# Performance work log

Measured on AMD Instinct MI355X. Metric: run time of the kernel, lower is better.

The kernel has to match this reference:

```python
import jax, jax.numpy as jnp
import numpy as np

B, C, H, W = 2, 256, 64, 64
HEADS, DIM_HEAD = 8, 64
INNER = HEADS * DIM_HEAD


def setup_inputs() -> dict:
    key = jax.random.key(0)
    k1, k2, k3, k4 = jax.random.split(key, 4)
    x = jax.random.normal(k1, (B, C, H, W), dtype=jnp.float32)
    # 1x1 conv weights stored as [out_ch, in_ch]
    w_qkv = jax.random.normal(k2, (3 * INNER, C), dtype=jnp.float32) * (1.0 / np.sqrt(C))
    w_out = jax.random.normal(k3, (C, INNER), dtype=jnp.float32) * (1.0 / np.sqrt(INNER))
    b_out = jax.random.normal(k4, (C,), dtype=jnp.float32) * 0.01
    return {"x": x, "w_qkv": w_qkv, "w_out": w_out, "b_out": b_out}


def reference(x, w_qkv, w_out, b_out):
    b, c, h, w = x.shape
    n = h * w
    # 1x1 conv == channel matmul
    qkv = jnp.einsum('oc,bchw->bohw', w_qkv, x)  # [B, 3*inner, H, W]
    qkv = qkv.reshape(b, 3, HEADS, DIM_HEAD, n)
    qkv = jnp.transpose(qkv, (1, 0, 2, 4, 3))    # [3, B, heads, N, dim_head]
    q, k, v = qkv[0], qkv[1], qkv[2]
    scale = 1.0 / (DIM_HEAD ** 0.5)
    dots = jnp.einsum('bhnd,bhmd->bhnm', q, k) * scale  # [B, heads, N, N]
    attn = jax.nn.softmax(dots, axis=-1)
    out = jnp.einsum('bhnm,bhmd->bhnd', attn, v)        # [B, heads, N, dim_head]
    out = jnp.transpose(out, (0, 1, 3, 2)).reshape(b, INNER, h, w)
    return jnp.einsum('ci,bihw->bchw', w_out, out) + b_out[None, :, None, None]
```

## Files before the change

kernel.cpp:

```cpp
#include <hip/hip_runtime.h>
#include <hip/hip_bf16.h>

typedef unsigned short u16;
typedef __attribute__((ext_vector_type(8))) short bf16x8;
typedef __attribute__((ext_vector_type(4))) float f32x4;
typedef __attribute__((ext_vector_type(8))) unsigned short u16x8;
typedef __attribute__((ext_vector_type(4))) unsigned short u16x4;

#define N_POS 4096
#define HEADS 8
#define DHEAD 64
#define CIN   256
#define INNER 512
#define NSPLIT 2
#define JCHUNK (N_POS / NSPLIT)

__device__ __forceinline__ u16 f2bf(float f) {
    union { float f; unsigned int u; } v; v.f = f;
    unsigned int u = v.u + 0x7FFFu + ((v.u >> 16) & 1u);
    return (u16)(u >> 16);
}

__device__ __forceinline__ float bf2f(u16 h) {
    union { float f; unsigned int u; } v; v.u = ((unsigned int)h) << 16;
    return v.f;
}

__device__ __forceinline__ unsigned int pkbf2(float lo, float hi) {
    union { __hip_bfloat162 b; unsigned int u; } cv;
    cv.b = __float22bfloat162_rn(make_float2(lo, hi));
    return cv.u;
}

__global__ __launch_bounds__(256) void k0_prep(const float* __restrict__ x,
                                               const float* __restrict__ w_qkv,
                                               const float* __restrict__ w_out,
                                               u16* __restrict__ xT,
                                               u16* __restrict__ wq,
                                               u16* __restrict__ wo) {
    int bid = blockIdx.x;
    int t   = threadIdx.x;
    if (bid < 256) {
        int b = bid >> 7, rest = bid & 127;
        int n  = (rest & 15) * 256 + t;
        int c0 = (rest >> 4) * 32;
        const float* xp = x + (size_t)b * CIN * N_POS + n;
        u16* op = xT + ((size_t)(b * N_POS + n)) * CIN + c0;
        for (int g = 0; g < 4; ++g) {
            u16x8 v;
            for (int j = 0; j < 8; ++j)
                v[j] = f2bf(xp[(size_t)(c0 + g * 8 + j) * N_POS]);
            *(u16x8*)(op + g * 8) = v;
        }
    } else if (bid < 448) {
        size_t idx = (size_t)(bid - 256) * 2048 + t * 8;
        u16x8 v;
        for (int j = 0; j < 8; ++j) v[j] = f2bf(w_qkv[idx + j]);
        *(u16x8*)(wq + idx) = v;
    } else {
        size_t idx = (size_t)(bid - 448) * 2048 + t * 8;
        u16x8 v;
        for (int j = 0; j < 8; ++j) v[j] = f2bf(w_out[idx + j]);
        *(u16x8*)(wo + idx) = v;
    }
}

__global__ __launch_bounds__(256, 2) void k1_qkv(const u16* __restrict__ wq,
                                                 const u16* __restrict__ xT,
                                                 u16* __restrict__ q_ws,
                                                 u16* __restrict__ k_ws,
                                                 u16* __restrict__ vt_ws) {
    __shared__ u16 Alds[64 * 40];
    __shared__ u16 Blds[256 * 40];
    int tid = threadIdx.x;
    int n0  = blockIdx.x * 256;
    int by  = blockIdx.y;
    int b   = blockIdx.z;
    int o0  = by * 64;
    int sel = by >> 3;
    int h   = by & 7;
    int wv = tid >> 6, l = tid & 63, quad = l >> 4, l15 = l & 15;
    int srow = tid >> 2, sseg = tid & 3;

    f32x4 acc[16] = {};
    for (int c0 = 0; c0 < CIN; c0 += 32) {
        *(u16x8*)&Alds[srow * 40 + sseg * 8] =
            *(const u16x8*)(wq + (size_t)(o0 + srow) * CIN + c0 + sseg * 8);
        const u16* xp = xT + ((size_t)(b * N_POS + n0 + tid)) * CIN + c0;
        u16* bd = &Blds[tid * 40];
        *(u16x8*)(bd)      = *(const u16x8*)(xp);
        *(u16x8*)(bd + 8)  = *(const u16x8*)(xp + 8);
        *(u16x8*)(bd + 16) = *(const u16x8*)(xp + 16);
        *(u16x8*)(bd + 24) = *(const u16x8*)(xp + 24);
        __syncthreads();
        bf16x8 af = *(const bf16x8*)&Alds[(wv * 16 + l15) * 40 + quad * 8];
        if (sel < 2) {
            for (int nt = 0; nt < 16; ++nt) {
                bf16x8 bfrag = *(const bf16x8*)&Blds[(nt * 16 + l15) * 40 + quad * 8];
                acc[nt] = __builtin_amdgcn_mfma_f32_16x16x32_bf16(af, bfrag, acc[nt], 0, 0, 0);
            }
        } else {
            for (int nt = 0; nt < 16; ++nt) {
                bf16x8 bfrag = *(const bf16x8*)&Blds[(nt * 16 + l15) * 40 + quad * 8];
                acc[nt] = __builtin_amdgcn_mfma_f32_16x16x32_bf16(bfrag, af, acc[nt], 0, 0, 0);
            }
        }
        __syncthreads();
    }
    const float QSCALE = 0.125f * 1.44269504088896f;
    int bh = b * HEADS + h;
    if (sel < 2) {
        float sc = (sel == 0) ? QSCALE : 1.0f;
        u16* base = (sel == 0) ? q_ws : k_ws;
        int dbase = wv * 16 + quad * 4;
        for (int nt = 0; nt < 16; ++nt) {
            int n = n0 + nt * 16 + l15;
            u16x4 pk;
            for (int r = 0; r < 4; ++r) pk[r] = f2bf(acc[nt][r] * sc);
            *(u16x4*)&base[((size_t)bh * N_POS + n) * DHEAD + dbase] = pk;
        }
    } else {
        int dloc = wv * 16 + l15;
        for (int nt = 0; nt < 16; ++nt) {
            u16x4 pk;
            for (int r = 0; r < 4; ++r) pk[r] = f2bf(acc[nt][r]);
            *(u16x4*)&vt_ws[((size_t)bh * DHEAD + dloc) * N_POS
                            + n0 + nt * 16 + quad * 4] = pk;
        }
    }
}

__global__ __launch_bounds__(256, 2) void k2_attn(const u16* __restrict__ q_ws,
                                                  const u16* __restrict__ k_ws,
                                                  const u16* __restrict__ vt_ws,
                                                  u16* __restrict__ op_ws,
                                                  float* __restrict__ lw_ws) {
    __shared__ u16 Klds[2][64 * 72];
    __shared__ u16 Vlds[2][64 * 72];
    int tid = threadIdx.x;
    int v   = blockIdx.x + (blockIdx.y << 4) + (blockIdx.z << 8);
    int slot = v & 7, idx = v >> 3;
    int bh   = slot * 2 + (idx & 1);
    int q0   = ((idx >> 1) & 15) * 256;
    int half = idx >> 5;
    int jbase = half * JCHUNK;
    int wv = tid >> 6, l = tid & 63, quad = l >> 4, l15 = l & 15;
    int srow = tid >> 2, sseg = tid & 3;
    int srowp = (srow & 0x23) | ((srow & 4) << 2) | ((srow & 0x18) >> 1);
    int kofs = srowp * 72 + sseg * 16;
    int vofs = srow * 72 + sseg * 16;

    const u16* qp = q_ws + ((size_t)(bh * N_POS + q0 + wv * 64 + l15)) * DHEAD + quad * 8;
    bf16x8 bq[4][2];
    for (int it = 0; it < 4; ++it) {
        bq[it][0] = *(const bf16x8*)(qp + (size_t)it * 16 * DHEAD);
        bq[it][1] = *(const bf16x8*)(qp + (size_t)it * 16 * DHEAD + 32);
    }

    f32x4 Oacc[4][4] = {};
    float lsum[4] = {0.f, 0.f, 0.f, 0.f};

    const u16* kp = k_ws + ((size_t)(bh * N_POS + srow)) * DHEAD + sseg * 16;
    const u16* vp = vt_ws + ((size_t)(bh * DHEAD + srow)) * N_POS + sseg * 16;

    u16x8 pf0 = *(const u16x8*)(kp + (size_t)jbase * DHEAD);
    u16x8 pf1 = *(const u16x8*)(kp + (size_t)jbase * DHEAD + 8);
    u16x8 pf2 = *(const u16x8*)(vp + jbase);
    u16x8 pf3 = *(const u16x8*)(vp + jbase + 8);
    *(u16x8*)&Klds[0][kofs]     = pf0;
    *(u16x8*)&Klds[0][kofs + 8] = pf1;
    *(u16x8*)&Vlds[0][vofs]     = pf2;
    *(u16x8*)&Vlds[0][vofs + 8] = pf3;
    {
        const u16* kpj = kp + (size_t)(jbase + 64) * DHEAD;
        pf0 = *(const u16x8*)kpj;
        pf1 = *(const u16x8*)(kpj + 8);
        pf2 = *(const u16x8*)(vp + jbase + 64);
        pf3 = *(const u16x8*)(vp + jbase + 72);
    }
    __syncthreads();

    int cur = 0;
    for (int j0 = jbase; j0 < jbase + JCHUNK; j0 += 64) {
        if (j0 + 64 < jbase + JCHUNK) {
            *(u16x8*)&Klds[cur ^ 1][kofs]     = pf0;
            *(u16x8*)&Klds[cur ^ 1][kofs + 8] = pf1;
            *(u16x8*)&Vlds[cur ^ 1][vofs]     = pf2;
            *(u16x8*)&Vlds[cur ^ 1][vofs + 8] = pf3;
        }

        union PF { unsigned int u[4]; bf16x8 v; };
        PF pfr[4][2];
        for (int p = 0; p < 2; ++p)
            for (int a = 0; a < 2; ++a) {
                const u16* kb = &Klds[cur][((2 * p + a) * 16 + l15) * 72 + quad * 8];
                bf16x8 kf0 = *(const bf16x8*)kb;
                bf16x8 kf1 = *(const bf16x8*)(kb + 32);
                f32x4 z[4];
                __builtin_amdgcn_s_setprio(1);
                for (int it = 0; it < 4; ++it) {
                    f32x4 t = {};
                    t = __builtin_amdgcn_mfma_f32_16x16x32_bf16(kf0, bq[it][0], t, 0, 0, 0);
                    t = __builtin_amdgcn_mfma_f32_16x16x32_bf16(kf1, bq[it][1], t, 0, 0, 0);
                    z[it] = t;
                }
                __builtin_amdgcn_s_setprio(0);
                for (int it = 0; it < 4; ++it) {
                    float e0 = __builtin_amdgcn_exp2f(z[it][0]);
                    float e1 = __builtin_amdgcn_exp2f(z[it][1]);
                    float e2 = __builtin_amdgcn_exp2f(z[it][2]);
                    float e3 = __builtin_amdgcn_exp2f(z[it][3]);
                    lsum[it] += (e0 + e1) + (e2 + e3);
                    pfr[it][p].u[2 * a]     = pkbf2(e0, e1);
                    pfr[it][p].u[2 * a + 1] = pkbf2(e2, e3);
                }
            }

        __builtin_amdgcn_s_setprio(1);
        for (int dt = 0; dt < 4; ++dt)
            for (int p = 0; p < 2; ++p) {
                bf16x8 vf = *(const bf16x8*)&Vlds[cur][(dt * 16 + l15) * 72 + p * 32 + quad * 8];
                for (int it = 0; it < 4; ++it)
                    Oacc[it][dt] = __builtin_amdgcn_mfma_f32_16x16x32_bf16(vf, pfr[it][p].v, Oacc[it][dt], 0, 0, 0);
            }
        __builtin_amdgcn_s_setprio(0);

        if (j0 + 128 < jbase + JCHUNK) {
            const u16* kpj = kp + (size_t)(j0 + 128) * DHEAD;
            pf0 = *(const u16x8*)kpj;
            pf1 = *(const u16x8*)(kpj + 8);
            pf2 = *(const u16x8*)(vp + j0 + 128);
            pf3 = *(const u16x8*)(vp + j0 + 136);
        }
        __syncthreads();
        cur ^= 1;
    }

    int b = bh >> 3, h = bh & 7;
    u16* opb = op_ws + (size_t)half * 2 * N_POS * INNER;
    float* lwb = lw_ws + (size_t)half * 2 * HEADS * N_POS;
    for (int it = 0; it < 4; ++it) {
        float ls = lsum[it];
        ls += __shfl_xor(ls, 16);
        ls += __shfl_xor(ls, 32);
        int n = q0 + wv * 64 + it * 16 + l15;
        if (quad == 0) lwb[(size_t)bh * N_POS + n] = ls;
        u16* dst = opb + ((size_t)(b * N_POS + n)) * INNER + h * DHEAD;
        for (int dt = 0; dt < 4; ++dt) {
            u16x4 pk;
            for (int r = 0; r < 4; ++r) pk[r] = f2bf(Oacc[it][dt][r]);
            *(u16x4*)&dst[dt * 16 + quad * 4] = pk;
        }
    }
}

__global__ __launch_bounds__(512) void k3_out(const u16* __restrict__ wo,
                                              const float* __restrict__ b_out,
                                              const u16* __restrict__ op_ws,
                                              const float* __restrict__ lw_ws,
                                              float* __restrict__ out) {
    __shared__ u16 Alds[2][256 * 36];
    __shared__ u16 Blds[16 * 520];
    int tid = threadIdx.x;
    int n0 = blockIdx.x * 16;
    int b  = blockIdx.y;
    int wv = tid >> 6, l = tid & 63, quad = l >> 4, l15 = l & 15;

    {
        int i8 = tid & 63;
        int h  = i8 >> 3;
        for (int p = 0; p < 2; ++p) {
            int nl = p * 8 + (tid >> 6);
            int n = n0 + nl;
            size_t lidx = ((size_t)(b * HEADS + h)) * N_POS + n;
            float ls = lw_ws[lidx] + lw_ws[(size_t)2 * HEADS * N_POS + lidx];
            float inv = 1.0f / ls;
            size_t oidx = ((size_t)(b * N_POS + n)) * INNER + i8 * 8;
            u16x8 pv0 = *(const u16x8*)(op_ws + oidx);
            u16x8 pv1 = *(const u16x8*)(op_ws + (size_t)2 * N_POS * INNER + oidx);
            u16x8 vv;
            for (int k = 0; k < 8; ++k)
                vv[k] = f2bf((bf2f(pv0[k]) + bf2f(pv1[k])) * inv);
            *(u16x8*)&Blds[nl * 520 + i8 * 8] = vv;
        }
    }
    {
        int row = tid >> 1, seg = tid & 1;
        const u16* src = wo + (size_t)row * INNER + seg * 16;
        *(u16x8*)&Alds[0][row * 36 + seg * 16]     = *(const u16x8*)src;
        *(u16x8*)&Alds[0][row * 36 + seg * 16 + 8] = *(const u16x8*)(src + 8);
    }
    __syncthreads();

    f32x4 acc[2] = {};
    int cur = 0;
    for (int s = 0; s < 16; ++s) {
        if (s + 1 < 16) {
            int row = tid >> 1, seg = tid & 1;
            const u16* src = wo + (size_t)row * INNER + (s + 1) * 32 + seg * 16;
            *(u16x8*)&Alds[cur ^ 1][row * 36 + seg * 16]     = *(const u16x8*)src;
            *(u16x8*)&Alds[cur ^ 1][row * 36 + seg * 16 + 8] = *(const u16x8*)(src + 8);
        }
        for (int ac = 0; ac < 2; ++ac) {
            bf16x8 af = *(const bf16x8*)&Alds[cur][(wv * 32 + ac * 16 + l15) * 36 + quad * 8];
            bf16x8 bfrag = *(const bf16x8*)&Blds[l15 * 520 + s * 32 + quad * 8];
            acc[ac] = __builtin_amdgcn_mfma_f32_16x16x32_bf16(af, bfrag, acc[ac], 0, 0, 0);
        }
        __syncthreads();
        cur ^= 1;
    }
    for (int ac = 0; ac < 2; ++ac)
        for (int r = 0; r < 4; ++r) {
            int c = wv * 32 + ac * 16 + quad * 4 + r;
            out[((size_t)(b * CIN + c)) * N_POS + n0 + l15] = acc[ac][r] + b_out[c];
        }
}

extern "C" void kernel_launch(void* const* d_in, const int* in_sizes, int n_in,
                              void* d_out, int out_size, void* d_ws, size_t ws_size,
                              hipStream_t stream) {
    const float* x     = (const float*)d_in[0];
    const float* w_qkv = (const float*)d_in[1];
    const float* w_out = (const float*)d_in[2];
    const float* b_out = (const float*)d_in[3];
    float* out = (float*)d_out;

    u16* ws    = (u16*)d_ws;
    u16* xT    = ws;
    u16* q_ws  = xT   + (size_t)2 * N_POS * CIN;
    u16* k_ws  = q_ws + (size_t)2 * HEADS * N_POS * DHEAD;
    u16* vt_ws = k_ws + (size_t)2 * HEADS * N_POS * DHEAD;
    u16* wq_bf = vt_ws + (size_t)2 * HEADS * N_POS * DHEAD;
    u16* wo_bf = wq_bf + (size_t)3 * INNER * CIN;
    u16* op_ws = wo_bf + (size_t)CIN * INNER;
    float* lw_ws = (float*)(op_ws + (size_t)NSPLIT * 2 * N_POS * INNER);

    hipLaunchKernelGGL(k0_prep, dim3(512), dim3(256), 0, stream,
                       x, w_qkv, w_out, xT, wq_bf, wo_bf);
    hipLaunchKernelGGL(k1_qkv, dim3(16, 24, 2), dim3(256), 0, stream,
                       wq_bf, xT, q_ws, k_ws, vt_ws);
    hipLaunchKernelGGL(k2_attn, dim3(16, 16, NSPLIT), dim3(256), 0, stream,
                       q_ws, k_ws, vt_ws, op_ws, lw_ws);
    hipLaunchKernelGGL(k3_out, dim3(256, 2), dim3(512), 0, stream,
                       wo_bf, b_out, op_ws, lw_ws, out);
}
```

Baseline: 178.5 us.

## Fuse bf16 input conversion into QKV projection kernel and drop prep kernel

Removes the separate prep kernel that converted x, w_qkv and w_out to bf16 and transposed x. The QKV projection now reads fp32 x and w_qkv directly and packs them to bf16 while staging into LDS, and an extra grid row converts w_out. This saves a kernel launch and the write and reread of the transposed bf16 copy of x. In exchange each of the 24 output-row blocks re-reads and re-converts fp32 x, doubling the bytes read per tile, using strided per-channel loads.

After: 177.6 us. About the same (-0.5%).

```diff
diff --git a/kernel.cpp b/kernel.cpp
--- a/kernel.cpp
+++ b/kernel.cpp
@@ -32,66 +32,59 @@
     return cv.u;
 }
 
-__global__ __launch_bounds__(256) void k0_prep(const float* __restrict__ x,
-                                               const float* __restrict__ w_qkv,
-                                               const float* __restrict__ w_out,
-                                               u16* __restrict__ xT,
-                                               u16* __restrict__ wq,
-                                               u16* __restrict__ wo) {
-    int bid = blockIdx.x;
-    int t   = threadIdx.x;
-    if (bid < 256) {
-        int b = bid >> 7, rest = bid & 127;
-        int n  = (rest & 15) * 256 + t;
-        int c0 = (rest >> 4) * 32;
-        const float* xp = x + (size_t)b * CIN * N_POS + n;
-        u16* op = xT + ((size_t)(b * N_POS + n)) * CIN + c0;
-        for (int g = 0; g < 4; ++g) {
-            u16x8 v;
-            for (int j = 0; j < 8; ++j)
-                v[j] = f2bf(xp[(size_t)(c0 + g * 8 + j) * N_POS]);
-            *(u16x8*)(op + g * 8) = v;
-        }
-    } else if (bid < 448) {
-        size_t idx = (size_t)(bid - 256) * 2048 + t * 8;
-        u16x8 v;
-        for (int j = 0; j < 8; ++j) v[j] = f2bf(w_qkv[idx + j]);
-        *(u16x8*)(wq + idx) = v;
-    } else {
-        size_t idx = (size_t)(bid - 448) * 2048 + t * 8;
-        u16x8 v;
-        for (int j = 0; j < 8; ++j) v[j] = f2bf(w_out[idx + j]);
-        *(u16x8*)(wo + idx) = v;
-    }
-}
-
-__global__ __launch_bounds__(256, 2) void k1_qkv(const u16* __restrict__ wq,
-                                                 const u16* __restrict__ xT,
+__global__ __launch_bounds__(256, 2) void k1_qkv(const float* __restrict__ x,
+                                                 const float* __restrict__ w_qkv,
+                                                 const float* __restrict__ w_out,
                                                  u16* __restrict__ q_ws,
                                                  u16* __restrict__ k_ws,
-                                                 u16* __restrict__ vt_ws) {
+                                                 u16* __restrict__ vt_ws,
+                                                 u16* __restrict__ wo) {
     __shared__ u16 Alds[64 * 40];
     __shared__ u16 Blds[256 * 40];
     int tid = threadIdx.x;
-    int n0  = blockIdx.x * 256;
     int by  = blockIdx.y;
     int b   = blockIdx.z;
+
+    if (by == 24) {
+        size_t base = ((size_t)((b * 16 + blockIdx.x) * 256 + tid)) * 16;
+        const float* src = w_out + base;
+        union { unsigned int u[4]; u16x8 v; } o0, o1;
+        for (int j = 0; j < 4; ++j) o0.u[j] = pkbf2(src[2 * j],     src[2 * j + 1]);
+        for (int j = 0; j < 4; ++j) o1.u[j] = pkbf2(src[8 + 2 * j], src[9 + 2 * j]);
+        *(u16x8*)(wo + base)     = o0.v;
+        *(u16x8*)(wo + base + 8) = o1.v;
+        return;
+    }
+
+    int n0  = blockIdx.x * 256;
     int o0  = by * 64;
     int sel = by >> 3;
     int h   = by & 7;
     int wv = tid >> 6, l = tid & 63, quad = l >> 4, l15 = l & 15;
     int srow = tid >> 2, sseg = tid & 3;
 
+    const float* xb = x + (size_t)b * CIN * N_POS + n0 + tid;
+
     f32x4 acc[16] = {};
     for (int c0 = 0; c0 < CIN; c0 += 32) {
-        *(u16x8*)&Alds[srow * 40 + sseg * 8] =
-            *(const u16x8*)(wq + (size_t)(o0 + srow) * CIN + c0 + sseg * 8);
-        const u16* xp = xT + ((size_t)(b * N_POS + n0 + tid)) * CIN + c0;
-        u16* bd = &Blds[tid * 40];
-        *(u16x8*)(bd)      = *(const u16x8*)(xp);
-        *(u16x8*)(bd + 8)  = *(const u16x8*)(xp + 8);
-        *(u16x8*)(bd + 16) = *(const u16x8*)(xp + 16);
-        *(u16x8*)(bd + 24) = *(const u16x8*)(xp + 24);
+        {
+            const float* wqp = w_qkv + (size_t)(o0 + srow) * CIN + c0 + sseg * 8;
+            union { unsigned int u[4]; u16x8 v; } av;
+            for (int j = 0; j < 4; ++j) av.u[j] = pkbf2(wqp[2 * j], wqp[2 * j + 1]);
+            *(u16x8*)&Alds[srow * 40 + sseg * 8] = av.v;
+        }
+        {
+            union { unsigned int u[16]; } tmp;
+            #pragma unroll
+            for (int j = 0; j < 16; ++j)
+                tmp.u[j] = pkbf2(xb[(size_t)(c0 + 2 * j) * N_POS],
+                                 xb[(size_t)(c0 + 2 * j + 1) * N_POS]);
+            u16* bd = &Blds[tid * 40];
+            *(u16x8*)(bd)      = *(u16x8*)&tmp.u[0];
+            *(u16x8*)(bd + 8)  = *(u16x8*)&tmp.u[4];
+            *(u16x8*)(bd + 16) = *(u16x8*)&tmp.u[8];
+            *(u16x8*)(bd + 24) = *(u16x8*)&tmp.u[12];
+        }
         __syncthreads();
         bf16x8 af = *(const bf16x8*)&Alds[(wv * 16 + l15) * 40 + quad * 8];
         if (sel < 2) {
@@ -326,19 +319,15 @@
     float* out = (float*)d_out;
 
     u16* ws    = (u16*)d_ws;
-    u16* xT    = ws;
-    u16* q_ws  = xT   + (size_t)2 * N_POS * CIN;
+    u16* q_ws  = ws;
     u16* k_ws  = q_ws + (size_t)2 * HEADS * N_POS * DHEAD;
     u16* vt_ws = k_ws + (size_t)2 * HEADS * N_POS * DHEAD;
-    u16* wq_bf = vt_ws + (size_t)2 * HEADS * N_POS * DHEAD;
-    u16* wo_bf = wq_bf + (size_t)3 * INNER * CIN;
+    u16* wo_bf = vt_ws + (size_t)2 * HEADS * N_POS * DHEAD;
     u16* op_ws = wo_bf + (size_t)CIN * INNER;
     float* lw_ws = (float*)(op_ws + (size_t)NSPLIT * 2 * N_POS * INNER);
 
-    hipLaunchKernelGGL(k0_prep, dim3(512), dim3(256), 0, stream,
-                       x, w_qkv, w_out, xT, wq_bf, wo_bf);
-    hipLaunchKernelGGL(k1_qkv, dim3(16, 24, 2), dim3(256), 0, stream,
-                       wq_bf, xT, q_ws, k_ws, vt_ws);
+    hipLaunchKernelGGL(k1_qkv, dim3(16, 25, 2), dim3(256), 0, stream,
+                       x, w_qkv, w_out, q_ws, k_ws, vt_ws, wo_bf);
     hipLaunchKernelGGL(k2_attn, dim3(16, 16, NSPLIT), dim3(256), 0, stream,
                        q_ws, k_ws, vt_ws, op_ws, lw_ws);
     hipLaunchKernelGGL(k3_out, dim3(256, 2), dim3(512), 0, stream,
```
